# Kernel optimization log

Hardware: AMD Instinct MI355X
Metric: run time of the kernel (lower is better)

## Reference

```python
import jax, jax.numpy as jnp
import numpy as np

LN_EPS = 1e-5
ALPHA_Q = 1.0

def _ln(t, g, b):
    mu = jnp.mean(t, -1, keepdims=True)
    var = jnp.var(t, -1, keepdims=True)
    return (t - mu) / jnp.sqrt(var + LN_EPS) * g + b

def _mlp(t, w1, b1, w2, b2):
    h = jax.nn.gelu(t @ w1.T + b1, approximate=False)
    return h @ w2.T + b2

def setup_inputs() -> dict:
    key = jax.random.key(0)
    B, N, L, E, H, D = 2, 2048, 2048, 1024, 16, 4
    ks = jax.random.split(key, 40)
    rn = lambda i, shape, sc: jax.random.normal(ks[i], shape, jnp.float32) * sc
    inp = {}
    inp['x'] = rn(0, (B, N, E), 1.0)
    inp['xp'] = jax.random.uniform(ks[1], (B, N, D), jnp.float32)
    inp['y'] = rn(2, (B, L, E), 1.0)
    inp['yp'] = jax.random.uniform(ks[3], (B, L, D), jnp.float32)
    inp['attn_mask'] = jax.random.uniform(ks[4], (1, 1, N, L), jnp.float32)
    # PositionEncoder params (torch Linear convention: weight [out,in])
    inp['p_w1'] = rn(5, (E, D), 1.0 / D)
    inp['p_b1'] = jax.random.uniform(ks[6], (E,), jnp.float32, 0.0, np.pi)
    inp['p_w2'] = rn(7, (E, D), 1.0 / D)
    inp['p_b2'] = jax.random.uniform(ks[8], (E,), jnp.float32, 0.0, np.pi)
    # QueryEncoder: LayerNorm + mlp1 + mlp2 (mlp0 is dead code in the source)
    inp['q_ln_g'] = jnp.ones((E,), jnp.float32); inp['q_ln_b'] = jnp.zeros((E,), jnp.float32)
    inp['q_m1_w1'] = rn(9, (2 * E, E), 0.02); inp['q_m1_b1'] = jnp.zeros((2 * E,), jnp.float32)
    inp['q_m1_w2'] = rn(10, (E, 2 * E), 0.02); inp['q_m1_b2'] = jnp.zeros((E,), jnp.float32)
    inp['q_m2_w1'] = rn(11, (2 * E, E), 0.02); inp['q_m2_b1'] = jnp.zeros((2 * E,), jnp.float32)
    inp['q_m2_w2'] = rn(12, (E, 2 * E), 0.02); inp['q_m2_b2'] = jnp.zeros((E,), jnp.float32)
    # KeyEncoder: LayerNorm + mlp1 (mlp0 dead code)
    inp['k_ln_g'] = jnp.ones((E,), jnp.float32); inp['k_ln_b'] = jnp.zeros((E,), jnp.float32)
    inp['k_m1_w1'] = rn(13, (2 * E, E), 0.02); inp['k_m1_b1'] = jnp.zeros((2 * E,), jnp.float32)
    inp['k_m1_w2'] = rn(14, (E, 2 * E), 0.02); inp['k_m1_b2'] = jnp.zeros((E,), jnp.float32)
    # V: LayerNorm + Linear
    inp['v_ln_g'] = jnp.ones((E,), jnp.float32); inp['v_ln_b'] = jnp.zeros((E,), jnp.float32)
    inp['v_w'] = rn(15, (E, E), 0.02); inp['v_b'] = jnp.zeros((E,), jnp.float32)
    # output projections
    inp['proj1_w'] = rn(16, (E, E), 0.02); inp['proj1_b'] = jnp.zeros((E,), jnp.float32)
    inp['proj2_w'] = rn(17, (E, D * H), 0.02); inp['proj2_b'] = jnp.zeros((E,), jnp.float32)
    return inp

def reference(x, xp, y, yp, attn_mask, p_w1, p_b1, p_w2, p_b2,
              q_ln_g, q_ln_b, q_m1_w1, q_m1_b1, q_m1_w2, q_m1_b2,
              q_m2_w1, q_m2_b1, q_m2_w2, q_m2_b2,
              k_ln_g, k_ln_b, k_m1_w1, k_m1_b1, k_m1_w2, k_m1_b2,
              v_ln_g, v_ln_b, v_w, v_b, proj1_w, proj1_b, proj2_w, proj2_b):
    B, N, E = x.shape
    L = y.shape[1]
    D = xp.shape[2]
    H = proj2_w.shape[1] // D
    C = E // H
    # PositionEncoder: query side with bias, key side without bias
    pxt = ALPHA_Q * xp
    xp1 = pxt @ p_w1.T + p_b1            # [B,N,E]
    xp2 = pxt @ p_w2.T + p_b2
    pyt = ALPHA_Q * yp
    yp1 = pyt @ p_w1.T                   # [B,L,E], no bias
    yp2 = pyt @ p_w2.T
    rh = lambda t: t.reshape(t.shape[0], -1, H, C)
    # QueryEncoder
    xn = _ln(x, q_ln_g, q_ln_b)
    x1 = _mlp(xn, q_m1_w1, q_m1_b1, q_m1_w2, q_m1_b2)
    x2 = _mlp(xn, q_m2_w1, q_m2_b1, q_m2_w2, q_m2_b2)
    q = jnp.concatenate([rh(x1 * jnp.cos(xp1)), rh(x1 * jnp.sin(xp1)),
                         rh(x2 * jnp.cos(xp2)), rh(x2 * jnp.sin(xp2))], axis=-1)  # [B,N,H,4C]
    # KeyEncoder (note: second cos/sin block is the raw position code)
    yn = _ln(y, k_ln_g, k_ln_b)
    y1 = _mlp(yn, k_m1_w1, k_m1_b1, k_m1_w2, k_m1_b2)
    k = jnp.concatenate([rh(y1 * jnp.cos(yp1)), rh(y1 * jnp.sin(yp1)),
                         rh(jnp.cos(yp2)), rh(jnp.sin(yp2))], axis=-1)            # [B,L,H,4C]
    scale = (4 * C) ** (-0.5)
    attn = jax.nn.softmax(jnp.einsum('bnhd,blhd->bhnl', q, k) * scale, axis=-1)
    # masked renormalization (mask applied AFTER softmax)
    eps = min(1e-8, 1.0 / L)
    attn = attn * attn_mask
    attn = attn / (jnp.sum(attn, axis=-1, keepdims=True) + eps)
    # values
    v = (_ln(y, v_ln_g, v_ln_b) @ v_w.T + v_b).reshape(B, L, H, C)
    out1 = jnp.einsum('bhnl,blhc->bnhc', attn, v).reshape(B, N, E) @ proj1_w.T + proj1_b
    out2 = jnp.einsum('bhnl,bld->bnhd', attn, yp) - xp[:, :, None, :]             # [B,N,H,D]
    out2 = out2.reshape(B, N, H * D) @ proj2_w.T + proj2_b
    return (out1 + out2, attn, xp)
```

## Files before the change

### kernel.cpp

```cpp
#include <hip/hip_runtime.h>
#include <math.h>
#include <stdint.h>

#define DEV static __device__ __forceinline__

typedef __bf16 bf16x8 __attribute__((ext_vector_type(8)));
typedef __bf16 bf16x4v __attribute__((ext_vector_type(4)));
typedef float f32x4 __attribute__((ext_vector_type(4)));

constexpr int Nn = 2048, Ll = 2048, Ee = 1024, Hh = 16;
constexpr float SCALE = 0.0625f;

constexpr size_t OFF_XN   = 0;
constexpr size_t OFF_YNK  = 8388608;
constexpr size_t OFF_YNV  = 16777216;
constexpr size_t OFF_H12  = 25165824;
constexpr size_t OFF_H3   = 58720256;
constexpr size_t OFF_X1   = 75497472;
constexpr size_t OFF_X2   = 83886080;
constexpr size_t OFF_Y1   = 92274688;
constexpr size_t OFF_QWS  = 100663296;
constexpr size_t OFF_KWS  = 134217728;
constexpr size_t OFF_VWS  = 167772160;
constexpr size_t OFF_DNV  = 176160768;
constexpr size_t OFF_YPT  = 176422912;
constexpr size_t OFF_MSK  = 176685056;
constexpr size_t OFF_AVZ  = 185073664;
constexpr size_t OFF_W1122= 193986560;
constexpr size_t OFF_W12  = 202375168;
constexpr size_t OFF_W22  = 206569472;
constexpr size_t OFF_WK1  = 210763776;
constexpr size_t OFF_WK2  = 214958080;
constexpr size_t OFF_WV   = 219152384;
constexpr size_t OFF_WP   = 221249536;
constexpr size_t OFF_EM   = 223477760;

DEV void gl2l(const void* g, void* l) {
  __builtin_amdgcn_global_load_lds((const __attribute__((address_space(1))) void*)g,
                                   (__attribute__((address_space(3))) void*)l, 16, 0, 0);
}

DEV float gelu_f(float v) {
  float x = v * 0.70710678118654752f;
  float ax = fabsf(x);
  float t = 1.f / fmaf(0.3275911f, ax, 1.f);
  float y = t * fmaf(t, fmaf(t, fmaf(t, fmaf(t, 1.061405429f, -1.453152027f),
                                     1.421413741f), -0.284496736f), 0.254829592f);
  float er = 1.f - y * __expf(-x * x);
  er = (x < 0.f) ? -er : er;
  return 0.5f * v * (1.f + er);
}

__launch_bounds__(256)
__global__ void prep_all(const float* __restrict__ s0, const float* __restrict__ s1,
                         const float* __restrict__ s2, const float* __restrict__ s3,
                         const float* __restrict__ s4, const float* __restrict__ s5,
                         const float* __restrict__ s6,
                         __bf16* __restrict__ d0, __bf16* __restrict__ d1,
                         __bf16* __restrict__ d2, __bf16* __restrict__ d3,
                         __bf16* __restrict__ d4, __bf16* __restrict__ d5,
                         __bf16* __restrict__ d6,
                         const float* __restrict__ pw1, const float* __restrict__ pw2,
                         __bf16* __restrict__ wp,
                         const float* __restrict__ mask, __bf16* __restrict__ mb,
                         const float* __restrict__ yp, __bf16* __restrict__ ypT) {
  int u = blockIdx.x * 256 + threadIdx.x;
  if (u < 3407872) {
    int seg = u >> 19, r = u & 524287;
    const float* s; __bf16* d;
    if      (seg == 0) { s = s0; d = d0; }
    else if (seg == 1) { s = s1; d = d1; }
    else if (seg == 2) { s = s2; d = d2; }
    else if (seg == 3) { s = s3; d = d3; }
    else if (seg == 4) { s = s4; d = d4; }
    else if (seg == 5) { s = s5; d = d5; }
    else               { s = s6; d = d6; }
    float4 v = ((const float4*)s)[r];
    bf16x4v o; o[0]=(__bf16)v.x; o[1]=(__bf16)v.y; o[2]=(__bf16)v.z; o[3]=(__bf16)v.w;
    ((bf16x4v*)d)[r] = o;
  } else if (u < 3686400) {
    int p = u - 3407872;
    int row = p / 272, c4 = p - row * 272;
    float4 v = (c4 < 256) ? ((const float4*)pw1)[row * 256 + c4]
                          : ((const float4*)pw2)[row * 16 + (c4 - 256)];
    bf16x4v o; o[0]=(__bf16)v.x; o[1]=(__bf16)v.y; o[2]=(__bf16)v.z; o[3]=(__bf16)v.w;
    *(bf16x4v*)(wp + (size_t)row * 1088 + (c4 << 2)) = o;
  } else if (u < 4734976) {
    int q = u - 3686400;
    float4 v = ((const float4*)mask)[q];
    bf16x4v o; o[0]=(__bf16)v.x; o[1]=(__bf16)v.y; o[2]=(__bf16)v.z; o[3]=(__bf16)v.w;
    ((bf16x4v*)mb)[q] = o;
  } else {
    int t0 = (u - 4734976) << 2;
    #pragma unroll
    for (int k = 0; k < 4; k++) {
      int i = t0 + k;
      int b = i >> 13, d = (i >> 11) & 3, l = i & 2047;
      ypT[i] = (__bf16)yp[(((size_t)b << 11) + l) * 4 + d];
    }
  }
}

__launch_bounds__(256)
__global__ void ln_all(const float* __restrict__ x, const float* __restrict__ y,
                       const float* __restrict__ qg, const float* __restrict__ qb,
                       const float* __restrict__ kg, const float* __restrict__ kb,
                       const float* __restrict__ vg, const float* __restrict__ vb,
                       __bf16* __restrict__ xn, __bf16* __restrict__ ynk,
                       __bf16* __restrict__ ynv) {
  const int t = blockIdx.x, tid = threadIdx.x;
  const bool isx = t < 4096;
  const int row = isx ? t : t - 4096;
  const float* src = (isx ? x : y) + (size_t)row * Ee;
  const float4 v = ((const float4*)src)[tid];
  float s = v.x + v.y + v.z + v.w;
  float q = v.x*v.x + v.y*v.y + v.z*v.z + v.w*v.w;
  #pragma unroll
  for (int o = 32; o > 0; o >>= 1) { s += __shfl_down(s, o); q += __shfl_down(q, o); }
  __shared__ float ls[4], lq[4];
  if ((tid & 63) == 0) { ls[tid >> 6] = s; lq[tid >> 6] = q; }
  __syncthreads();
  s = ls[0] + ls[1] + ls[2] + ls[3];
  q = lq[0] + lq[1] + lq[2] + lq[3];
  const float mu = s * (1.f / Ee);
  const float rstd = rsqrtf(q * (1.f / Ee) - mu * mu + 1e-5f);
  const int e0 = tid << 2;
  float h0 = (v.x - mu) * rstd, h1 = (v.y - mu) * rstd,
        h2 = (v.z - mu) * rstd, h3 = (v.w - mu) * rstd;
  if (isx) {
    bf16x4v o;
    o[0] = (__bf16)(h0 * qg[e0]   + qb[e0]);
    o[1] = (__bf16)(h1 * qg[e0+1] + qb[e0+1]);
    o[2] = (__bf16)(h2 * qg[e0+2] + qb[e0+2]);
    o[3] = (__bf16)(h3 * qg[e0+3] + qb[e0+3]);
    *(bf16x4v*)(xn + (size_t)row * Ee + e0) = o;
  } else {
    bf16x4v ok, ov;
    ok[0] = (__bf16)(h0 * kg[e0]   + kb[e0]);
    ok[1] = (__bf16)(h1 * kg[e0+1] + kb[e0+1]);
    ok[2] = (__bf16)(h2 * kg[e0+2] + kb[e0+2]);
    ok[3] = (__bf16)(h3 * kg[e0+3] + kb[e0+3]);
    ov[0] = (__bf16)(h0 * vg[e0]   + vb[e0]);
    ov[1] = (__bf16)(h1 * vg[e0+1] + vb[e0+1]);
    ov[2] = (__bf16)(h2 * vg[e0+2] + vb[e0+2]);
    ov[3] = (__bf16)(h3 * vg[e0+3] + vb[e0+3]);
    *(bf16x4v*)(ynk + (size_t)row * Ee + e0) = ok;
    *(bf16x4v*)(ynv + (size_t)row * Ee + e0) = ov;
  }
}

#define GEMM256_CORE(A_, lda_, W_, ldw_, K_)                                          \
  const int w = tid >> 6, lane = tid & 63, g = lane >> 4, li = lane & 15;             \
  const int wm = (w >> 2) << 7, wn = (w & 3) << 6;                                    \
  f32x4 acc[8][4];                                                                    \
  _Pragma("unroll")                                                                   \
  for (int i = 0; i < 8; i++)                                                         \
    _Pragma("unroll")                                                                 \
    for (int j = 0; j < 4; j++) acc[i][j] = (f32x4)0.f;                               \
  auto stage = [&](int buf, int kt) {                                                 \
    const int col0 = kt << 5;                                                         \
    _Pragma("unroll")                                                                 \
    for (int jj = 0; jj < 2; jj++) {                                                  \
      int c = (jj << 9) + tid;                                                        \
      int row = c >> 2, sl = c & 3;                                                   \
      int col = col0 + ((sl ^ (row & 3)) << 3);                                       \
      gl2l(A_ + (size_t)(m0 + row) * lda_ + col, As[buf] + ((c - lane) << 3));        \
      gl2l(W_ + (size_t)(n0 + row) * ldw_ + col, Bs[buf] + ((c - lane) << 3));        \
    }                                                                                 \
  };                                                                                  \
  const int NT = (K_) >> 5;                                                           \
  stage(0, 0);                                                                        \
  for (int kt = 0; kt < NT; kt++) {                                                   \
    const int cur = kt & 1;                                                           \
    if (kt + 1 < NT) {                                                                \
      stage(cur ^ 1, kt + 1);                                                         \
      asm volatile("s_waitcnt vmcnt(4)" ::: "memory");                                \
    } else {                                                                          \
      asm volatile("s_waitcnt vmcnt(0)" ::: "memory");                                \
    }                                                                                 \
    __builtin_amdgcn_s_barrier();                                                     \
    __builtin_amdgcn_sched_barrier(0);                                                \
    bf16x8 af[8], bw[4];                                                              \
    _Pragma("unroll")                                                                 \
    for (int i = 0; i < 8; i++) {                                                     \
      int ra = wm + (i << 4) + li;                                                    \
      af[i] = *(const bf16x8*)(As[cur] + ra * 32 + ((g ^ (ra & 3)) << 3));            \
    }                                                                                 \
    _Pragma("unroll")                                                                 \
    for (int j = 0; j < 4; j++) {                                                     \
      int rb = wn + (j << 4) + li;                                                    \
      bw[j] = *(const bf16x8*)(Bs[cur] + rb * 32 + ((g ^ (rb & 3)) << 3));            \
    }                                                                                 \
    _Pragma("unroll")                                                                 \
    for (int i = 0; i < 8; i++)                                                       \
      _Pragma("unroll")                                                               \
      for (int j = 0; j < 4; j++)                                                     \
        acc[i][j] = __builtin_amdgcn_mfma_f32_16x16x32_bf16(af[i], bw[j], acc[i][j], 0, 0, 0); \
    asm volatile("s_waitcnt lgkmcnt(0)" ::: "memory");                                \
    __builtin_amdgcn_sched_barrier(0);                                                \
    __builtin_amdgcn_s_barrier();                                                     \
  }

__launch_bounds__(512, 2)
__global__ void gemm_mlp1(const __bf16* __restrict__ xn, const __bf16* __restrict__ ynk,
                          const __bf16* __restrict__ w1122, const __bf16* __restrict__ wk1,
                          const float* __restrict__ qb1, const float* __restrict__ qb2,
                          const float* __restrict__ kb1,
                          __bf16* __restrict__ h12, __bf16* __restrict__ h3) {
  __shared__ __align__(16) __bf16 As[2][256 * 32];
  __shared__ __align__(16) __bf16 Bs[2][256 * 32];
  const int tid = threadIdx.x, bid = blockIdx.x;
  const bool seg1 = bid >= 256;
  const __bf16* A; const __bf16* W; __bf16* out; int m0, n0, ldc;
  if (!seg1) { A = xn;  W = w1122; out = h12; ldc = 4096; m0 = (bid >> 4) << 8; n0 = (bid & 15) << 8; }
  else { int rr = bid - 256; A = ynk; W = wk1; out = h3; ldc = 2048; m0 = (rr >> 3) << 8; n0 = (rr & 7) << 8; }
  GEMM256_CORE(A, 1024, W, 1024, 1024)
  #pragma unroll
  for (int j = 0; j < 4; j++) {
    int n = n0 + wn + (j << 4) + li;
    float bias = seg1 ? kb1[n] : ((n < 2048) ? qb1[n] : qb2[n - 2048]);
    #pragma unroll
    for (int i = 0; i < 8; i++) {
      #pragma unroll
      for (int r = 0; r < 4; r++) {
        int m = m0 + wm + (i << 4) + (g << 2) + r;
        out[(size_t)m * ldc + n] = (__bf16)gelu_f(acc[i][j][r] + bias);
      }
    }
  }
}

__launch_bounds__(512, 2)
__global__ void gemm_mlp2(const __bf16* __restrict__ h12, const __bf16* __restrict__ h3,
                          const __bf16* __restrict__ ynv,
                          const __bf16* __restrict__ w12, const __bf16* __restrict__ w22,
                          const __bf16* __restrict__ wk2, const __bf16* __restrict__ wv,
                          const float* __restrict__ bx1, const float* __restrict__ bx2,
                          const float* __restrict__ by1, const float* __restrict__ bv,
                          __bf16* __restrict__ x1, __bf16* __restrict__ x2,
                          __bf16* __restrict__ y1, __bf16* __restrict__ vT) {
  __shared__ __align__(16) __bf16 As[2][256 * 32];
  __shared__ __align__(16) __bf16 Bs[2][256 * 32];
  const int tid = threadIdx.x, bid = blockIdx.x;
  const int seg = bid >> 6, rr = bid & 63;
  const int m0 = (rr >> 2) << 8, n0 = (rr & 3) << 8;
  const __bf16* A; const __bf16* W; const float* bias; __bf16* out; int lda, K;
  if      (seg == 0) { A = h12;        lda = 4096; W = w12; bias = bx1; out = x1; K = 2048; }
  else if (seg == 1) { A = h12 + 2048; lda = 4096; W = w22; bias = bx2; out = x2; K = 2048; }
  else if (seg == 2) { A = h3;         lda = 2048; W = wk2; bias = by1; out = y1; K = 2048; }
  else               { A = ynv;        lda = 1024; W = wv;  bias = bv;  out = vT; K = 1024; }
  GEMM256_CORE(A, lda, W, K, K)
  #pragma unroll
  for (int j = 0; j < 4; j++) {
    int n = n0 + wn + (j << 4) + li;
    float bs = bias[n];
    #pragma unroll
    for (int i = 0; i < 8; i++) {
      #pragma unroll
      for (int r = 0; r < 4; r++) {
        int m = m0 + wm + (i << 4) + (g << 2) + r;
        float v = acc[i][j][r] + bs;
        if (seg == 3) {
          int bb = m >> 11, l = m & 2047, hh = n >> 6, cc = n & 63;
          vT[(((size_t)(bb * Hh + hh) * 64 + cc) << 11) + l] = (__bf16)v;
        } else {
          out[(size_t)m * 1024 + n] = (__bf16)v;
        }
      }
    }
  }
}

__launch_bounds__(256)
__global__ void build_qk(const __bf16* __restrict__ x1, const __bf16* __restrict__ x2,
                         const float* __restrict__ xp,
                         const __bf16* __restrict__ y1, const float* __restrict__ yp,
                         const float* __restrict__ pw1, const float* __restrict__ pb1,
                         const float* __restrict__ pw2, const float* __restrict__ pb2,
                         __bf16* __restrict__ q_ws, __bf16* __restrict__ k_ws) {
  const bool isq = blockIdx.x < 2048;
  const int bid = isq ? blockIdx.x : blockIdx.x - 2048;
  const int t = (bid << 1) + (threadIdx.x >> 7);
  const int tl = threadIdx.x & 127;
  const int b = t >> 11, n = t & 2047;
  const int hh = tl >> 3, ch = tl & 7;
  const int e0 = (hh << 6) + (ch << 3);
  const float* pos = isq ? xp : yp;
  const float p0 = pos[(size_t)t*4], p1 = pos[(size_t)t*4+1],
              p2 = pos[(size_t)t*4+2], p3 = pos[(size_t)t*4+3];
  bf16x8 o0, o1, o2, o3;
  if (isq) {
    bf16x8 v1 = *(const bf16x8*)(x1 + (size_t)t * Ee + e0);
    bf16x8 v2 = *(const bf16x8*)(x2 + (size_t)t * Ee + e0);
    #pragma unroll
    for (int sub = 0; sub < 8; sub++) {
      int e = e0 + sub;
      float a1 = pw1[e*4]*p0 + pw1[e*4+1]*p1 + pw1[e*4+2]*p2 + pw1[e*4+3]*p3 + pb1[e];
      float a2 = pw2[e*4]*p0 + pw2[e*4+1]*p1 + pw2[e*4+2]*p2 + pw2[e*4+3]*p3 + pb2[e];
      float s1, c1, s2, c2;
      __sincosf(a1, &s1, &c1); __sincosf(a2, &s2, &c2);
      float xv1 = (float)v1[sub], xv2 = (float)v2[sub];
      o0[sub] = (__bf16)(xv1 * c1); o1[sub] = (__bf16)(xv1 * s1);
      o2[sub] = (__bf16)(xv2 * c2); o3[sub] = (__bf16)(xv2 * s2);
    }
  } else {
    bf16x8 v1 = *(const bf16x8*)(y1 + (size_t)t * Ee + e0);
    #pragma unroll
    for (int sub = 0; sub < 8; sub++) {
      int e = e0 + sub;
      float a1 = pw1[e*4]*p0 + pw1[e*4+1]*p1 + pw1[e*4+2]*p2 + pw1[e*4+3]*p3;
      float a2 = pw2[e*4]*p0 + pw2[e*4+1]*p1 + pw2[e*4+2]*p2 + pw2[e*4+3]*p3;
      float s1, c1, s2, c2;
      __sincosf(a1, &s1, &c1); __sincosf(a2, &s2, &c2);
      float yv = (float)v1[sub];
      o0[sub] = (__bf16)(yv * c1); o1[sub] = (__bf16)(yv * s1);
      o2[sub] = (__bf16)c2;        o3[sub] = (__bf16)s2;
    }
  }
  const int k = n & 7, bc = ch ^ k;
  __bf16* base = (isq ? q_ws : k_ws) + ((((size_t)b * Hh + hh) * Nn + n) << 8);
  *(bf16x8*)(base + ((bc          ) << 3)) = o0;
  *(bf16x8*)(base + (((8  ^ k) ^ ch) << 3)) = o1;
  *(bf16x8*)(base + (((16 ^ k) ^ ch) << 3)) = o2;
  *(bf16x8*)(base + (((24 ^ k) ^ ch) << 3)) = o3;
}

__launch_bounds__(512, 1)
__global__ void attn_fused(const __bf16* __restrict__ q_ws, const __bf16* __restrict__ k_ws,
                           const __bf16* __restrict__ vT_ws, const __bf16* __restrict__ ypT_g,
                           const __bf16* __restrict__ mask_bf, const float* __restrict__ xp,
                           __bf16* __restrict__ em_g, float* __restrict__ dinv_g,
                           __bf16* __restrict__ avz) {
  __shared__ __align__(16) __bf16 kq[2][32 * 256];
  __shared__ __align__(16) __bf16 ms[2][256 * 32];
  __shared__ __align__(16) __bf16 vt[2][64 * 40];
  __shared__ __align__(16) __bf16 pT[256 * 40];
  __shared__ __align__(16) __bf16 ypl[2][16 * 40];
  const int tid = threadIdx.x, w = tid >> 6, lane = tid & 63, g = lane >> 4, li = lane & 15;
  const int logical = ((blockIdx.x & 7) << 5) + (blockIdx.x >> 3);
  const int bh = logical >> 3, nt = logical & 7;
  const int b = bh >> 4, h = bh & 15;
  const int n0 = nt << 8;
  const __bf16* qb = q_ws + (((size_t)bh * Nn + n0) << 8);
  const __bf16* kb = k_ws + (((size_t)bh * Ll) << 8);
  const __bf16* vb = vT_ws + ((size_t)bh << 17);
  const __bf16* yb = ypT_g + ((size_t)b << 13);
  const __bf16* mb = mask_bf + ((size_t)n0 << 11);

  bf16x8 aq[2][8];
  #pragma unroll
  for (int rf = 0; rf < 2; rf++) {
    const int nloc = (w << 5) + (rf << 4) + li;
    #pragma unroll
    for (int s = 0; s < 8; s++)
      aq[rf][s] = *(const bf16x8*)(qb + ((size_t)nloc << 8) + ((((s << 2) + g) ^ (nloc & 7)) << 3));
  }
  for (int i = tid; i < 960; i += 512) {
    int buf = i / 480, idx = i - buf * 480;
    ypl[buf][160 + idx] = (__bf16)0.f;
  }
  {
    const int vc = tid >> 3, vl = (tid & 7) << 2;
    bf16x4v vreg = *(const bf16x4v*)(vb + ((size_t)vc << 11) + vl);
    bf16x4v ypreg;
    if (tid < 32) ypreg = *(const bf16x4v*)(yb + ((size_t)(tid >> 3) << 11) + ((tid & 7) << 2));
    #pragma unroll
    for (int j = 0; j < 2; j++) {
      int c = (j << 9) + tid;
      gl2l(kb + (size_t)(c >> 5) * 256 + ((c & 31) << 3), kq[0] + ((c - lane) << 3));
      gl2l(mb + (size_t)(c >> 2) * 2048 + ((c & 3) << 3), ms[0] + ((c - lane) << 3));
    }
    *(bf16x4v*)(vt[0] + vc * 40 + vl) = vreg;
    if (tid < 32) *(bf16x4v*)(ypl[0] + (tid >> 3) * 40 + ((tid & 7) << 2)) = ypreg;
  }
  __syncthreads();

  float se[2][4], te[2][4];
  f32x4 accv[2][4], accp[2];
  #pragma unroll
  for (int rf = 0; rf < 2; rf++) {
    #pragma unroll
    for (int r = 0; r < 4; r++) { se[rf][r] = 0.f; te[rf][r] = 0.f; }
    #pragma unroll
    for (int cb = 0; cb < 4; cb++) accv[rf][cb] = (f32x4)0.f;
    accp[rf] = (f32x4)0.f;
  }

  for (int t = 0; t < 64; ++t) {
    const int l0 = t << 5, cur = t & 1, nxt = cur ^ 1;
    const bool more = (t < 63);
    bf16x4v vreg, ypreg;
    if (more) {
      const int l1 = l0 + 32;
      vreg = *(const bf16x4v*)(vb + ((size_t)(tid >> 3) << 11) + l1 + ((tid & 7) << 2));
      if (tid < 32) ypreg = *(const bf16x4v*)(yb + ((size_t)(tid >> 3) << 11) + l1 + ((tid & 7) << 2));
      #pragma unroll
      for (int j = 0; j < 2; j++) {
        int c = (j << 9) + tid;
        gl2l(kb + (size_t)(l1 + (c >> 5)) * 256 + ((c & 31) << 3), kq[nxt] + ((c - lane) << 3));
        gl2l(mb + (size_t)(c >> 2) * 2048 + l1 + ((c & 3) << 3), ms[nxt] + ((c - lane) << 3));
      }
    }
    f32x4 Cs[2][2];
    Cs[0][0] = (f32x4)0.f; Cs[0][1] = (f32x4)0.f; Cs[1][0] = (f32x4)0.f; Cs[1][1] = (f32x4)0.f;
    #pragma unroll
    for (int lb = 0; lb < 2; lb++) {
      const int kr = (lb << 4) + li;
      #pragma unroll
      for (int s = 0; s < 8; s++) {
        bf16x8 bk = *(const bf16x8*)(kq[cur] + kr * 256 + ((((s << 2) + g) ^ (kr & 7)) << 3));
        Cs[0][lb] = __builtin_amdgcn_mfma_f32_16x16x32_bf16(aq[0][s], bk, Cs[0][lb], 0, 0, 0);
        Cs[1][lb] = __builtin_amdgcn_mfma_f32_16x16x32_bf16(aq[1][s], bk, Cs[1][lb], 0, 0, 0);
      }
    }
    #pragma unroll
    for (int rf = 0; rf < 2; rf++) {
      #pragma unroll
      for (int lb = 0; lb < 2; lb++) {
        #pragma unroll
        for (int r = 0; r < 4; r++) {
          const int row = (w << 5) + (rf << 4) + (g << 2) + r;
          float e = __expf(Cs[rf][lb][r] * SCALE);
          float mkv = (float)ms[cur][row * 32 + (lb << 4) + li];
          float em = e * mkv;
          se[rf][r] += e; te[rf][r] += em;
          pT[row * 40 + (lb << 4) + li] = (__bf16)em;
        }
      }
    }
    asm volatile("s_waitcnt lgkmcnt(0)" ::: "memory");
    __builtin_amdgcn_sched_barrier(0);
    #pragma unroll
    for (int j = 0; j < 2; j++) {
      int q = (j << 6) + lane;
      int row = q >> 2, ch = q & 3;
      bf16x8 pv = *(const bf16x8*)(pT + ((w << 5) + row) * 40 + (ch << 3));
      *(bf16x8*)(em_g + ((size_t)bh << 22) + ((size_t)(n0 + (w << 5) + row) << 11) + l0 + (ch << 3)) = pv;
    }
    bf16x8 vv[4];
    #pragma unroll
    for (int cb = 0; cb < 4; cb++)
      vv[cb] = *(const bf16x8*)(vt[cur] + ((cb << 4) + li) * 40 + (g << 3));
    bf16x8 yy = *(const bf16x8*)(ypl[cur] + li * 40 + (g << 3));
    #pragma unroll
    for (int rf = 0; rf < 2; rf++) {
      bf16x8 pa = *(const bf16x8*)(pT + ((w << 5) + (rf << 4) + li) * 40 + (g << 3));
      #pragma unroll
      for (int cb = 0; cb < 4; cb++)
        accv[rf][cb] = __builtin_amdgcn_mfma_f32_16x16x32_bf16(pa, vv[cb], accv[rf][cb], 0, 0, 0);
      accp[rf] = __builtin_amdgcn_mfma_f32_16x16x32_bf16(pa, yy, accp[rf], 0, 0, 0);
    }
    if (more) {
      *(bf16x4v*)(vt[nxt] + (tid >> 3) * 40 + ((tid & 7) << 2)) = vreg;
      if (tid < 32) *(bf16x4v*)(ypl[nxt] + (tid >> 3) * 40 + ((tid & 7) << 2)) = ypreg;
    }
    __syncthreads();
  }

  #pragma unroll
  for (int rf = 0; rf < 2; rf++) {
    #pragma unroll
    for (int r = 0; r < 4; r++) {
      float s = se[rf][r], tt = te[rf][r];
      #pragma unroll
      for (int o = 1; o < 16; o <<= 1) { s += __shfl_xor(s, o); tt += __shfl_xor(tt, o); }
      float dinv = 1.f / (tt + 1e-8f * s);
      const int n = n0 + (w << 5) + (rf << 4) + (g << 2) + r;
      if (li == 0) dinv_g[((size_t)bh << 11) + n] = dinv;
      #pragma unroll
      for (int cb = 0; cb < 4; cb++)
        avz[((size_t)b * Nn + n) * 1088 + (h << 6) + (cb << 4) + li] = (__bf16)(accv[rf][cb][r] * dinv);
      if (li < 4) {
        float z = accp[rf][r] * dinv - xp[(((size_t)b * Nn + n) << 2) + li];
        avz[((size_t)b * Nn + n) * 1088 + 1024 + (h << 2) + li] = (__bf16)z;
      }
    }
  }
}

__launch_bounds__(256)
__global__ void fin_proj(const __bf16* __restrict__ A, const __bf16* __restrict__ W,
                         const float* __restrict__ bias1, const float* __restrict__ bias2,
                         float* __restrict__ out,
                         const __bf16* __restrict__ em_g, const float* __restrict__ dinv_g,
                         float* __restrict__ attn_out,
                         const float* __restrict__ xp, float* __restrict__ xp_out) {
  constexpr int N = 1024, K = 1088;
  __shared__ __align__(16) __bf16 As[2][128 * 32];
  __shared__ __align__(16) __bf16 Bs[2][64 * 32];
  const int tid = threadIdx.x;
  if (blockIdx.x >= 512) {
    const int sbid = blockIdx.x - 512;
    if (sbid < 64) {
      int idx = sbid * 256 + tid;
      ((float4*)xp_out)[idx] = ((const float4*)xp)[idx];
    }
    for (size_t i8 = sbid * 256ul + tid; i8 < 16777216ul; i8 += 524288ul) {
      bf16x8 v = ((const bf16x8*)em_g)[i8];
      float dv = dinv_g[i8 >> 8];
      float4 o0, o1;
      o0.x = (float)v[0] * dv; o0.y = (float)v[1] * dv; o0.z = (float)v[2] * dv; o0.w = (float)v[3] * dv;
      o1.x = (float)v[4] * dv; o1.y = (float)v[5] * dv; o1.z = (float)v[6] * dv; o1.w = (float)v[7] * dv;
      ((float4*)attn_out)[i8 * 2]     = o0;
      ((float4*)attn_out)[i8 * 2 + 1] = o1;
    }
    return;
  }
  const int w = tid >> 6, lane = tid & 63, g = lane >> 4, li = lane & 15;
  const int bt = blockIdx.x >> 4;
  const int m0 = bt << 7, n0 = (blockIdx.x & 15) << 6;
  const int wm = (w >> 1) << 6, wn = (w & 1) << 5;
  f32x4 acc[4][2];
  #pragma unroll
  for (int i = 0; i < 4; i++) { acc[i][0] = (f32x4)0.f; acc[i][1] = (f32x4)0.f; }
  auto stage = [&](int buf, int kt) {
    const int col0 = kt << 5;
    #pragma unroll
    for (int j = 0; j < 2; j++) {
      int c = (j << 8) + tid;
      int row = c >> 2, sl = c & 3;
      int col = col0 + ((sl ^ (row & 3)) << 3);
      gl2l(A + (size_t)(m0 + row) * K + col, As[buf] + ((c - lane) << 3));
    }
    {
      int c = tid;
      int row = c >> 2, sl = c & 3;
      int col = col0 + ((sl ^ (row & 3)) << 3);
      gl2l(W + (size_t)(n0 + row) * K + col, Bs[buf] + ((c - lane) << 3));
    }
  };
  const int NT = K >> 5;
  stage(0, 0);
  for (int kt = 0; kt < NT; kt++) {
    const int cur = kt & 1;
    if (kt + 1 < NT) {
      stage(cur ^ 1, kt + 1);
      asm volatile("s_waitcnt vmcnt(3)" ::: "memory");
    } else {
      asm volatile("s_waitcnt vmcnt(0)" ::: "memory");
    }
    __builtin_amdgcn_s_barrier();
    __builtin_amdgcn_sched_barrier(0);
    bf16x8 af[4], bw[2];
    #pragma unroll
    for (int i = 0; i < 4; i++) {
      int ra = wm + (i << 4) + li;
      af[i] = *(const bf16x8*)(As[cur] + ra * 32 + ((g ^ (ra & 3)) << 3));
    }
    #pragma unroll
    for (int j = 0; j < 2; j++) {
      int rb = wn + (j << 4) + li;
      bw[j] = *(const bf16x8*)(Bs[cur] + rb * 32 + ((g ^ (rb & 3)) << 3));
    }
    #pragma unroll
    for (int i = 0; i < 4; i++)
      #pragma unroll
      for (int j = 0; j < 2; j++)
        acc[i][j] = __builtin_amdgcn_mfma_f32_16x16x32_bf16(af[i], bw[j], acc[i][j], 0, 0, 0);
    asm volatile("s_waitcnt lgkmcnt(0)" ::: "memory");
    __builtin_amdgcn_sched_barrier(0);
    __builtin_amdgcn_s_barrier();
  }
  #pragma unroll
  for (int j = 0; j < 2; j++) {
    int n = n0 + wn + (j << 4) + li;
    float bias = bias1[n] + bias2[n];
    #pragma unroll
    for (int i = 0; i < 4; i++) {
      #pragma unroll
      for (int r = 0; r < 4; r++) {
        int m = m0 + wm + (i << 4) + (g << 2) + r;
        out[(size_t)m * N + n] = acc[i][j][r] + bias;
      }
    }
  }
}

extern "C" void kernel_launch(void* const* d_in, const int* in_sizes, int n_in,
                              void* d_out, int out_size, void* d_ws, size_t ws_size,
                              hipStream_t stream) {
  (void)in_sizes; (void)n_in; (void)out_size; (void)ws_size;
  const float* x       = (const float*)d_in[0];
  const float* xp      = (const float*)d_in[1];
  const float* y       = (const float*)d_in[2];
  const float* yp      = (const float*)d_in[3];
  const float* mask    = (const float*)d_in[4];
  const float* p_w1    = (const float*)d_in[5];
  const float* p_b1    = (const float*)d_in[6];
  const float* p_w2    = (const float*)d_in[7];
  const float* p_b2    = (const float*)d_in[8];
  const float* q_ln_g  = (const float*)d_in[9];
  const float* q_ln_b  = (const float*)d_in[10];
  const float* q_m1_w1 = (const float*)d_in[11];
  const float* q_m1_b1 = (const float*)d_in[12];
  const float* q_m1_w2 = (const float*)d_in[13];
  const float* q_m1_b2 = (const float*)d_in[14];
  const float* q_m2_w1 = (const float*)d_in[15];
  const float* q_m2_b1 = (const float*)d_in[16];
  const float* q_m2_w2 = (const float*)d_in[17];
  const float* q_m2_b2 = (const float*)d_in[18];
  const float* k_ln_g  = (const float*)d_in[19];
  const float* k_ln_b  = (const float*)d_in[20];
  const float* k_m1_w1 = (const float*)d_in[21];
  const float* k_m1_b1 = (const float*)d_in[22];
  const float* k_m1_w2 = (const float*)d_in[23];
  const float* k_m1_b2 = (const float*)d_in[24];
  const float* v_ln_g  = (const float*)d_in[25];
  const float* v_ln_b  = (const float*)d_in[26];
  const float* v_w     = (const float*)d_in[27];
  const float* v_b     = (const float*)d_in[28];
  const float* proj1_w = (const float*)d_in[29];
  const float* proj1_b = (const float*)d_in[30];
  const float* proj2_w = (const float*)d_in[31];
  const float* proj2_b = (const float*)d_in[32];

  char* ws = (char*)d_ws;
  __bf16* xn    = (__bf16*)(ws + OFF_XN);
  __bf16* ynk   = (__bf16*)(ws + OFF_YNK);
  __bf16* ynv   = (__bf16*)(ws + OFF_YNV);
  __bf16* h12   = (__bf16*)(ws + OFF_H12);
  __bf16* h3    = (__bf16*)(ws + OFF_H3);
  __bf16* x1    = (__bf16*)(ws + OFF_X1);
  __bf16* x2    = (__bf16*)(ws + OFF_X2);
  __bf16* y1    = (__bf16*)(ws + OFF_Y1);
  __bf16* q_ws  = (__bf16*)(ws + OFF_QWS);
  __bf16* k_ws  = (__bf16*)(ws + OFF_KWS);
  __bf16* vT_ws = (__bf16*)(ws + OFF_VWS);
  float*  dinv  = (float*)(ws + OFF_DNV);
  __bf16* ypT   = (__bf16*)(ws + OFF_YPT);
  __bf16* mskb  = (__bf16*)(ws + OFF_MSK);
  __bf16* avz   = (__bf16*)(ws + OFF_AVZ);
  __bf16* w1122 = (__bf16*)(ws + OFF_W1122);
  __bf16* w12   = (__bf16*)(ws + OFF_W12);
  __bf16* w22   = (__bf16*)(ws + OFF_W22);
  __bf16* wk1   = (__bf16*)(ws + OFF_WK1);
  __bf16* wk2   = (__bf16*)(ws + OFF_WK2);
  __bf16* wv    = (__bf16*)(ws + OFF_WV);
  __bf16* wp    = (__bf16*)(ws + OFF_WP);
  __bf16* em    = (__bf16*)(ws + OFF_EM);

  float* out0     = (float*)d_out;
  float* attn_out = out0 + (size_t)4194304;
  float* xp_out   = out0 + (size_t)138412032;

  prep_all<<<18512, 256, 0, stream>>>(q_m1_w1, q_m2_w1, q_m1_w2, q_m2_w2, k_m1_w1, k_m1_w2, v_w,
                                      w1122, w1122 + 2097152, w12, w22, wk1, wk2, wv,
                                      proj1_w, proj2_w, wp, mask, mskb, yp, ypT);
  ln_all<<<8192, 256, 0, stream>>>(x, y, q_ln_g, q_ln_b, k_ln_g, k_ln_b, v_ln_g, v_ln_b,
                                   xn, ynk, ynv);
  gemm_mlp1<<<384, 512, 0, stream>>>(xn, ynk, w1122, wk1, q_m1_b1, q_m2_b1, k_m1_b1, h12, h3);
  gemm_mlp2<<<256, 512, 0, stream>>>(h12, h3, ynv, w12, w22, wk2, wv,
                                     q_m1_b2, q_m2_b2, k_m1_b2, v_b, x1, x2, y1, vT_ws);
  build_qk<<<4096, 256, 0, stream>>>(x1, x2, xp, y1, yp, p_w1, p_b1, p_w2, p_b2, q_ws, k_ws);
  attn_fused<<<256, 512, 0, stream>>>(q_ws, k_ws, vT_ws, ypT, mskb, xp, em, dinv, avz);
  fin_proj<<<2560, 256, 0, stream>>>(avz, wp, proj1_b, proj2_b, out0,
                                     em, dinv, attn_out, xp, xp_out);
}
```

Measured before the change: 733.8 us.

## Deepen GEMM K-tile to 64 and split key MLP1 into 128-row tiles

Both MLP GEMM kernels now stage 64-wide K slices per iteration instead of 32, using an 8-way XOR swizzle and two MFMA sub-steps per tile. This halves the number of barrier/wait rounds per output tile. The key-encoder part of gemm_mlp1 uses 128-row tiles, which raises the grid from 384 to 512 blocks for better balance across CUs. In exchange, LDS per block doubles to 128KB, which likely allows only one 512-thread block per CU and reduces latency hiding.

```diff
diff --git a/kernel.cpp b/kernel.cpp
--- a/kernel.cpp
+++ b/kernel.cpp
@@ -149,53 +149,65 @@
   }
 }
 
-#define GEMM256_CORE(A_, lda_, W_, ldw_, K_)                                          \
+#define GEMM_CORE_BK64(BM_, A_, lda_, W_, ldw_, K_)                                   \
   const int w = tid >> 6, lane = tid & 63, g = lane >> 4, li = lane & 15;             \
-  const int wm = (w >> 2) << 7, wn = (w & 3) << 6;                                    \
-  f32x4 acc[8][4];                                                                    \
+  const int wm = (w >> 2) * (BM_ / 2), wn = (w & 3) << 6;                             \
+  constexpr int MI = BM_ / 32;                                                        \
+  f32x4 acc[MI][4];                                                                   \
   _Pragma("unroll")                                                                   \
-  for (int i = 0; i < 8; i++)                                                         \
+  for (int i = 0; i < MI; i++)                                                        \
     _Pragma("unroll")                                                                 \
     for (int j = 0; j < 4; j++) acc[i][j] = (f32x4)0.f;                               \
   auto stage = [&](int buf, int kt) {                                                 \
-    const int col0 = kt << 5;                                                         \
+    const int col0 = kt << 6;                                                         \
     _Pragma("unroll")                                                                 \
-    for (int jj = 0; jj < 2; jj++) {                                                  \
+    for (int jj = 0; jj < BM_ / 64; jj++) {                                           \
       int c = (jj << 9) + tid;                                                        \
-      int row = c >> 2, sl = c & 3;                                                   \
-      int col = col0 + ((sl ^ (row & 3)) << 3);                                       \
-      gl2l(A_ + (size_t)(m0 + row) * lda_ + col, As[buf] + ((c - lane) << 3));        \
-      gl2l(W_ + (size_t)(n0 + row) * ldw_ + col, Bs[buf] + ((c - lane) << 3));        \
+      int row = c >> 3, sl = c & 7;                                                   \
+      int col = col0 + ((sl ^ (row & 7)) << 3);                                       \
+      gl2l(A_ + (size_t)(m0 + row) * lda_ + col, (buf ? As1 : As0) + ((c - lane) << 3)); \
+    }                                                                                 \
+    _Pragma("unroll")                                                                 \
+    for (int jj = 0; jj < 4; jj++) {                                                  \
+      int c = (jj << 9) + tid;                                                        \
+      int row = c >> 3, sl = c & 7;                                                   \
+      int col = col0 + ((sl ^ (row & 7)) << 3);                                       \
+      gl2l(W_ + (size_t)(n0 + row) * ldw_ + col, (buf ? Bs1 : Bs0) + ((c - lane) << 3)); \
     }                                                                                 \
   };                                                                                  \
-  const int NT = (K_) >> 5;                                                           \
+  const int NT = (K_) >> 6;                                                           \
   stage(0, 0);                                                                        \
   for (int kt = 0; kt < NT; kt++) {                                                   \
     const int cur = kt & 1;                                                           \
     if (kt + 1 < NT) {                                                                \
       stage(cur ^ 1, kt + 1);                                                         \
-      asm volatile("s_waitcnt vmcnt(4)" ::: "memory");                                \
+      asm volatile("s_waitcnt vmcnt(%0)" :: "i"(BM_ / 64 + 4) : "memory");            \
     } else {                                                                          \
       asm volatile("s_waitcnt vmcnt(0)" ::: "memory");                                \
     }                                                                                 \
     __builtin_amdgcn_s_barrier();                                                     \
     __builtin_amdgcn_sched_barrier(0);                                                \
-    bf16x8 af[8], bw[4];                                                              \
+    const __bf16* Acur = cur ? As1 : As0;                                             \
+    const __bf16* Bcur = cur ? Bs1 : Bs0;                                             \
     _Pragma("unroll")                                                                 \
-    for (int i = 0; i < 8; i++) {                                                     \
-      int ra = wm + (i << 4) + li;                                                    \
-      af[i] = *(const bf16x8*)(As[cur] + ra * 32 + ((g ^ (ra & 3)) << 3));            \
+    for (int ks = 0; ks < 2; ks++) {                                                  \
+      bf16x8 af[MI], bw[4];                                                           \
+      _Pragma("unroll")                                                               \
+      for (int i = 0; i < MI; i++) {                                                  \
+        int ra = wm + (i << 4) + li;                                                  \
+        af[i] = *(const bf16x8*)(Acur + ra * 64 + ((((ks << 2) | g) ^ (ra & 7)) << 3)); \
+      }                                                                               \
+      _Pragma("unroll")                                                               \
+      for (int j = 0; j < 4; j++) {                                                   \
+        int rb = wn + (j << 4) + li;                                                  \
+        bw[j] = *(const bf16x8*)(Bcur + rb * 64 + ((((ks << 2) | g) ^ (rb & 7)) << 3)); \
+      }                                                                               \
+      _Pragma("unroll")                                                               \
+      for (int i = 0; i < MI; i++)                                                    \
+        _Pragma("unroll")                                                             \
+        for (int j = 0; j < 4; j++)                                                   \
+          acc[i][j] = __builtin_amdgcn_mfma_f32_16x16x32_bf16(af[i], bw[j], acc[i][j], 0, 0, 0); \
     }                                                                                 \
-    _Pragma("unroll")                                                                 \
-    for (int j = 0; j < 4; j++) {                                                     \
-      int rb = wn + (j << 4) + li;                                                    \
-      bw[j] = *(const bf16x8*)(Bs[cur] + rb * 32 + ((g ^ (rb & 3)) << 3));            \
-    }                                                                                 \
-    _Pragma("unroll")                                                                 \
-    for (int i = 0; i < 8; i++)                                                       \
-      _Pragma("unroll")                                                               \
-      for (int j = 0; j < 4; j++)                                                     \
-        acc[i][j] = __builtin_amdgcn_mfma_f32_16x16x32_bf16(af[i], bw[j], acc[i][j], 0, 0, 0); \
     asm volatile("s_waitcnt lgkmcnt(0)" ::: "memory");                                \
     __builtin_amdgcn_sched_barrier(0);                                                \
     __builtin_amdgcn_s_barrier();                                                     \
@@ -207,24 +219,42 @@
                           const float* __restrict__ qb1, const float* __restrict__ qb2,
                           const float* __restrict__ kb1,
                           __bf16* __restrict__ h12, __bf16* __restrict__ h3) {
-  __shared__ __align__(16) __bf16 As[2][256 * 32];
-  __shared__ __align__(16) __bf16 Bs[2][256 * 32];
+  __shared__ __align__(16) __bf16 As0[256 * 64];
+  __shared__ __align__(16) __bf16 As1[256 * 64];
+  __shared__ __align__(16) __bf16 Bs0[256 * 64];
+  __shared__ __align__(16) __bf16 Bs1[256 * 64];
   const int tid = threadIdx.x, bid = blockIdx.x;
-  const bool seg1 = bid >= 256;
-  const __bf16* A; const __bf16* W; __bf16* out; int m0, n0, ldc;
-  if (!seg1) { A = xn;  W = w1122; out = h12; ldc = 4096; m0 = (bid >> 4) << 8; n0 = (bid & 15) << 8; }
-  else { int rr = bid - 256; A = ynk; W = wk1; out = h3; ldc = 2048; m0 = (rr >> 3) << 8; n0 = (rr & 7) << 8; }
-  GEMM256_CORE(A, 1024, W, 1024, 1024)
-  #pragma unroll
-  for (int j = 0; j < 4; j++) {
-    int n = n0 + wn + (j << 4) + li;
-    float bias = seg1 ? kb1[n] : ((n < 2048) ? qb1[n] : qb2[n - 2048]);
-    #pragma unroll
-    for (int i = 0; i < 8; i++) {
-      #pragma unroll
-      for (int r = 0; r < 4; r++) {
-        int m = m0 + wm + (i << 4) + (g << 2) + r;
-        out[(size_t)m * ldc + n] = (__bf16)gelu_f(acc[i][j][r] + bias);
+  if (bid < 256) {
+    const int m0 = (bid >> 4) << 8, n0 = (bid & 15) << 8;
+    GEMM_CORE_BK64(256, xn, 1024, w1122, 1024, 1024)
+    #pragma unroll
+    for (int j = 0; j < 4; j++) {
+      int n = n0 + wn + (j << 4) + li;
+      float bias = (n < 2048) ? qb1[n] : qb2[n - 2048];
+      #pragma unroll
+      for (int i = 0; i < MI; i++) {
+        #pragma unroll
+        for (int r = 0; r < 4; r++) {
+          int m = m0 + wm + (i << 4) + (g << 2) + r;
+          h12[(size_t)m * 4096 + n] = (__bf16)gelu_f(acc[i][j][r] + bias);
+        }
+      }
+    }
+  } else {
+    const int rr = bid - 256;
+    const int m0 = (rr >> 3) << 7, n0 = (rr & 7) << 8;
+    GEMM_CORE_BK64(128, ynk, 1024, wk1, 1024, 1024)
+    #pragma unroll
+    for (int j = 0; j < 4; j++) {
+      int n = n0 + wn + (j << 4) + li;
+      float bias = kb1[n];
+      #pragma unroll
+      for (int i = 0; i < MI; i++) {
+        #pragma unroll
+        for (int r = 0; r < 4; r++) {
+          int m = m0 + wm + (i << 4) + (g << 2) + r;
+          h3[(size_t)m * 2048 + n] = (__bf16)gelu_f(acc[i][j][r] + bias);
+        }
       }
     }
   }
@@ -239,8 +269,10 @@
                           const float* __restrict__ by1, const float* __restrict__ bv,
                           __bf16* __restrict__ x1, __bf16* __restrict__ x2,
                           __bf16* __restrict__ y1, __bf16* __restrict__ vT) {
-  __shared__ __align__(16) __bf16 As[2][256 * 32];
-  __shared__ __align__(16) __bf16 Bs[2][256 * 32];
+  __shared__ __align__(16) __bf16 As0[256 * 64];
+  __shared__ __align__(16) __bf16 As1[256 * 64];
+  __shared__ __align__(16) __bf16 Bs0[256 * 64];
+  __shared__ __align__(16) __bf16 Bs1[256 * 64];
   const int tid = threadIdx.x, bid = blockIdx.x;
   const int seg = bid >> 6, rr = bid & 63;
   const int m0 = (rr >> 2) << 8, n0 = (rr & 3) << 8;
@@ -249,13 +281,13 @@
   else if (seg == 1) { A = h12 + 2048; lda = 4096; W = w22; bias = bx2; out = x2; K = 2048; }
   else if (seg == 2) { A = h3;         lda = 2048; W = wk2; bias = by1; out = y1; K = 2048; }
   else               { A = ynv;        lda = 1024; W = wv;  bias = bv;  out = vT; K = 1024; }
-  GEMM256_CORE(A, lda, W, K, K)
+  GEMM_CORE_BK64(256, A, lda, W, K, K)
   #pragma unroll
   for (int j = 0; j < 4; j++) {
     int n = n0 + wn + (j << 4) + li;
     float bs = bias[n];
     #pragma unroll
-    for (int i = 0; i < 8; i++) {
+    for (int i = 0; i < MI; i++) {
       #pragma unroll
       for (int r = 0; r < 4; r++) {
         int m = m0 + wm + (i << 4) + (g << 2) + r;
@@ -648,7 +680,7 @@
                                       proj1_w, proj2_w, wp, mask, mskb, yp, ypT);
   ln_all<<<8192, 256, 0, stream>>>(x, y, q_ln_g, q_ln_b, k_ln_g, k_ln_b, v_ln_g, v_ln_b,
                                    xn, ynk, ynv);
-  gemm_mlp1<<<384, 512, 0, stream>>>(xn, ynk, w1122, wk1, q_m1_b1, q_m2_b1, k_m1_b1, h12, h3);
+  gemm_mlp1<<<512, 512, 0, stream>>>(xn, ynk, w1122, wk1, q_m1_b1, q_m2_b1, k_m1_b1, h12, h3);
   gemm_mlp2<<<256, 512, 0, stream>>>(h12, h3, ynv, w12, w22, wk2, wv,
                                      q_m1_b2, q_m2_b2, k_m1_b2, v_b, x1, x2, y1, vT_ws);
   build_qk<<<4096, 256, 0, stream>>>(x1, x2, xp, y1, yp, p_w1, p_b1, p_w2, p_b2, q_ws, k_ws);
```

Measured after the change: 697.5 us. 4.9% less time.
